# Performance work log

Hardware: AMD Instinct MI355X
Metric: run time of the kernel (lower is better)

## Reference

```python
import jax, jax.numpy as jnp
import numpy as np

FACTOR = 5

def setup_inputs() -> dict:
    key = jax.random.key(0)
    kq, kk, kv, ki = jax.random.split(key, 4)
    B, L, H, D = 8, 2048, 8, 64
    u = FACTOR * int(np.ceil(np.log(L)))  # sample_k == n_top == 40
    return {
        "queries": jax.random.normal(kq, (B, L, H, D), dtype=jnp.float32),
        "keys": jax.random.normal(kk, (B, L, H, D), dtype=jnp.float32),
        "values": jax.random.normal(kv, (B, L, H, D), dtype=jnp.float32),
        "index_sample": jax.random.randint(ki, (L, u), 0, L, dtype=jnp.int32),
    }

def reference(queries, keys, values, index_sample):
    B, L, H, D = queries.shape
    # faithful to torch .view(B, H, -1, D) on contiguous tensors (a reshape, not a transpose)
    q = queries.reshape(B, H, L, D)
    k = keys.reshape(B, H, L, D)
    v = values.reshape(B, H, L, D)
    u = FACTOR * int(np.ceil(np.log(L)))  # U_part == u
    # --- _prob_QK: sample keys per query, score, pick top-u queries ---
    K_sample = k[:, :, index_sample, :]                      # [B,H,L,u,D] gather over L_K
    QK_sample = jnp.einsum('bhld,bhlsd->bhls', q, K_sample)  # [B,H,L,u]
    M = QK_sample.max(axis=-1) - QK_sample.sum(axis=-1) / L  # sparsity measure [B,H,L]
    M_top = jax.lax.top_k(M, u)[1]                           # [B,H,u] indices of active queries
    Q_reduce = jnp.take_along_axis(q, M_top[..., None], axis=2)  # [B,H,u,D]
    scores = jnp.einsum('bhud,bhld->bhul', Q_reduce, k)      # [B,H,u,L]
    scale = 1.0 / float(np.sqrt(D))
    attn = jax.nn.softmax(scores * scale, axis=-1)           # dropout is identity in eval
    context = jnp.einsum('bhul,bhld->bhud', attn, v)         # [B,H,u,D]
    return context, attn
```

## Files before the change

kernel.cpp:

```cpp
#include <hip/hip_runtime.h>
#include <math.h>

#define LSEQ 2048
#define DDIM 64
#define UU   40
#define NBH  64
#define CTX_ELEMS (NBH*UU*DDIM)

__global__ __launch_bounds__(256, 8) void k12_sample_m(
    const float* __restrict__ q, const float* __restrict__ k,
    const int* __restrict__ idxs, float* __restrict__ M, float* __restrict__ ctx) {
  int b = blockIdx.x;
  int bh = b & 63;
  int ltile = b >> 6;
  int t = threadIdx.x;
  int lid = t >> 4;
  int lane = t & 15;
  int l = ltile * 16 + lid;

  int gt = b * 256 + t;
  if (gt < CTX_ELEMS) ctx[gt] = 0.f;

  float4 qv = *(const float4*)(q + ((size_t)(bh * LSEQ + l)) * DDIM + lane * 4);
  const float* kbase = k + (size_t)bh * LSEQ * DDIM;
  const int4* ir = (const int4*)(idxs + l * UU);

  float mx = -INFINITY, sm = 0.f;
#pragma unroll 1
  for (int s4 = 0; s4 < UU / 4; ++s4) {
    int4 jv = ir[s4];
    float4 k0 = *(const float4*)(kbase + (size_t)jv.x * DDIM + lane * 4);
    float4 k1 = *(const float4*)(kbase + (size_t)jv.y * DDIM + lane * 4);
    float4 k2 = *(const float4*)(kbase + (size_t)jv.z * DDIM + lane * 4);
    float4 k3 = *(const float4*)(kbase + (size_t)jv.w * DDIM + lane * 4);
    float d0 = qv.x * k0.x + qv.y * k0.y + qv.z * k0.z + qv.w * k0.w;
    float d1 = qv.x * k1.x + qv.y * k1.y + qv.z * k1.z + qv.w * k1.w;
    float d2 = qv.x * k2.x + qv.y * k2.y + qv.z * k2.z + qv.w * k2.w;
    float d3 = qv.x * k3.x + qv.y * k3.y + qv.z * k3.z + qv.w * k3.w;
#pragma unroll
    for (int off = 1; off < 16; off <<= 1) {
      d0 += __shfl_xor(d0, off, 64);
      d1 += __shfl_xor(d1, off, 64);
      d2 += __shfl_xor(d2, off, 64);
      d3 += __shfl_xor(d3, off, 64);
    }
    mx = fmaxf(fmaxf(fmaxf(mx, d0), fmaxf(d1, d2)), d3);
    sm += (d0 + d1) + (d2 + d3);
  }
  if (lane == 0) M[bh * LSEQ + l] = mx - sm * (1.0f / (float)LSEQ);
}

__global__ __launch_bounds__(256) void k3_topk(const float* __restrict__ M,
                                               int* __restrict__ Mtop) {
  int bh = blockIdx.x;
  int t = threadIdx.x;
  int w = t >> 6;
  int lane = t & 63;
  float v[8];
#pragma unroll
  for (int j = 0; j < 8; ++j) v[j] = M[bh * LSEQ + t + 256 * j];
  __shared__ float swv[4];
  __shared__ int   swi[4];
  __shared__ int   win;
  for (int it = 0; it < UU; ++it) {
    float bv = -INFINITY; int bi = 0x7fffffff;
#pragma unroll
    for (int j = 0; j < 8; ++j) {
      if (v[j] > bv) { bv = v[j]; bi = t + 256 * j; }
    }
#pragma unroll
    for (int off = 32; off > 0; off >>= 1) {
      float ov = __shfl_xor(bv, off, 64);
      int   oi = __shfl_xor(bi, off, 64);
      if (ov > bv || (ov == bv && oi < bi)) { bv = ov; bi = oi; }
    }
    if (lane == 0) { swv[w] = bv; swi[w] = bi; }
    __syncthreads();
    if (t == 0) {
      float fv = swv[0]; int fi = swi[0];
#pragma unroll
      for (int j = 1; j < 4; ++j) {
        if (swv[j] > fv || (swv[j] == fv && swi[j] < fi)) { fv = swv[j]; fi = swi[j]; }
      }
      Mtop[bh * UU + it] = fi;
      win = fi;
    }
    __syncthreads();
    int wi = win;
    if ((wi & 255) == t) v[wi >> 8] = -INFINITY;
  }
}

__global__ __launch_bounds__(256, 4) void k4_scores(
    const float* __restrict__ q, const float* __restrict__ k,
    const int* __restrict__ Mtop, float* __restrict__ attn) {
  int b = blockIdx.x;
  int bh = b & 63;
  int chunk = (b >> 6) & 7;
  int u0 = (b >> 9) * 20;
  int l = chunk * 256 + threadIdx.x;
  const float4* kr = (const float4*)(k + (size_t)(bh * LSEQ + l) * DDIM);
  float4 kv[16];
#pragma unroll
  for (int i = 0; i < 16; ++i) kv[i] = kr[i];
  for (int u = u0; u < u0 + 20; ++u) {
    int qi = __builtin_amdgcn_readfirstlane(Mtop[bh * UU + u]);
    const float4* qr = (const float4*)(q + (size_t)(bh * LSEQ + qi) * DDIM);
    float a0 = 0.f, a1 = 0.f, a2 = 0.f, a3 = 0.f;
#pragma unroll
    for (int i = 0; i < 16; i += 4) {
      float4 x0 = qr[i], x1 = qr[i+1], x2 = qr[i+2], x3 = qr[i+3];
      float4 y0 = kv[i], y1 = kv[i+1], y2 = kv[i+2], y3 = kv[i+3];
      a0 += x0.x*y0.x + x0.y*y0.y + x0.z*y0.z + x0.w*y0.w;
      a1 += x1.x*y1.x + x1.y*y1.y + x1.z*y1.z + x1.w*y1.w;
      a2 += x2.x*y2.x + x2.y*y2.y + x2.z*y2.z + x2.w*y2.w;
      a3 += x3.x*y3.x + x3.y*y3.y + x3.z*y3.z + x3.w*y3.w;
    }
    attn[(size_t)(bh * UU + u) * LSEQ + l] = ((a0+a1)+(a2+a3)) * 0.125f;
  }
}

__global__ __launch_bounds__(256) void k5_softmax(float* __restrict__ attn) {
  __shared__ float red[256];
  int row = blockIdx.x;
  float* p = attn + (size_t)row * LSEQ;
  int t = threadIdx.x;
  float v[8];
  float mx = -INFINITY;
#pragma unroll
  for (int i = 0; i < 8; ++i) { v[i] = p[t + 256 * i]; mx = fmaxf(mx, v[i]); }
  red[t] = mx; __syncthreads();
  for (int off = 128; off > 0; off >>= 1) {
    if (t < off) red[t] = fmaxf(red[t], red[t + off]);
    __syncthreads();
  }
  mx = red[0]; __syncthreads();
  float sm = 0.f;
#pragma unroll
  for (int i = 0; i < 8; ++i) { v[i] = __expf(v[i] - mx); sm += v[i]; }
  red[t] = sm; __syncthreads();
  for (int off = 128; off > 0; off >>= 1) {
    if (t < off) red[t] += red[t + off];
    __syncthreads();
  }
  float inv = 1.0f / red[0];
#pragma unroll
  for (int i = 0; i < 8; ++i) p[t + 256 * i] = v[i] * inv;
}

__global__ __launch_bounds__(256) void k7_context(
    const float* __restrict__ attn, const float* __restrict__ v,
    float* __restrict__ ctx) {
  __shared__ float vt[256 * DDIM];
  int b = blockIdx.x;
  int bh = b & 63;
  int l0 = (b >> 6) * 256;
  int t = threadIdx.x;

  const float4* src = (const float4*)(v + ((size_t)bh * LSEQ + l0) * DDIM);
  float4* dst = (float4*)vt;
#pragma unroll
  for (int i = 0; i < 16; ++i) dst[t + 256 * i] = src[t + 256 * i];
  __syncthreads();

  int w = t >> 6;
  int d = t & 63;
  const float* ab = attn + ((size_t)bh * UU + w * 10) * LSEQ + l0;
  float acc[10];
#pragma unroll
  for (int u = 0; u < 10; ++u) acc[u] = 0.f;
#pragma unroll 1
  for (int l4 = 0; l4 < 64; ++l4) {
    int l = l4 * 4;
    float4 av[10];
#pragma unroll
    for (int u = 0; u < 10; ++u)
      av[u] = *(const float4*)(ab + (size_t)u * LSEQ + l);
#pragma unroll
    for (int i = 0; i < 4; ++i) {
      float vv = vt[(l + i) * DDIM + d];
#pragma unroll
      for (int u = 0; u < 10; ++u)
        acc[u] = fmaf(((const float*)&av[u])[i], vv, acc[u]);
    }
  }
#pragma unroll
  for (int u = 0; u < 10; ++u)
    atomicAdd(&ctx[((size_t)bh * UU + w * 10 + u) * DDIM + d], acc[u]);
}

extern "C" void kernel_launch(void* const* d_in, const int* in_sizes, int n_in,
                              void* d_out, int out_size, void* d_ws, size_t ws_size,
                              hipStream_t stream) {
  const float* q   = (const float*)d_in[0];
  const float* k   = (const float*)d_in[1];
  const float* v   = (const float*)d_in[2];
  const int*   idx = (const int*)d_in[3];

  float* ctx  = (float*)d_out;
  float* attn = (float*)d_out + CTX_ELEMS;

  float* M    = (float*)d_ws;
  int*   Mtop = (int*)(M + NBH * LSEQ);

  k12_sample_m<<<NBH * 128, 256, 0, stream>>>(q, k, idx, M, ctx);
  k3_topk<<<NBH, 256, 0, stream>>>(M, Mtop);
  k4_scores<<<NBH * 16, 256, 0, stream>>>(q, k, Mtop, attn);
  k5_softmax<<<NBH * UU, 256, 0, stream>>>(attn);
  k7_context<<<NBH * 8, 256, 0, stream>>>(attn, v, ctx);
}
```

Measured before the change: 312.3 us.

## Fuse scores, softmax and context into one kernel using LDS-resident scores

```diff
diff --git a/kernel.cpp b/kernel.cpp
--- a/kernel.cpp
+++ b/kernel.cpp
@@ -9,7 +9,7 @@
 
 __global__ __launch_bounds__(256, 8) void k12_sample_m(
     const float* __restrict__ q, const float* __restrict__ k,
-    const int* __restrict__ idxs, float* __restrict__ M, float* __restrict__ ctx) {
+    const int* __restrict__ idxs, float* __restrict__ M) {
   int b = blockIdx.x;
   int bh = b & 63;
   int ltile = b >> 6;
@@ -17,9 +17,6 @@
   int lid = t >> 4;
   int lane = t & 15;
   int l = ltile * 16 + lid;
-
-  int gt = b * 256 + t;
-  if (gt < CTX_ELEMS) ctx[gt] = 0.f;
 
   float4 qv = *(const float4*)(q + ((size_t)(bh * LSEQ + l)) * DDIM + lane * 4);
   const float* kbase = k + (size_t)bh * LSEQ * DDIM;
@@ -91,102 +88,193 @@
   }
 }
 
-__global__ __launch_bounds__(256, 4) void k4_scores(
+__global__ __launch_bounds__(256, 2) void k457_fused(
     const float* __restrict__ q, const float* __restrict__ k,
-    const int* __restrict__ Mtop, float* __restrict__ attn) {
+    const float* __restrict__ v, const int* __restrict__ Mtop,
+    float* __restrict__ attn, float* __restrict__ ctx) {
+  __shared__ float sct[LSEQ * 8];
+  __shared__ float red[32 * 64];
+  __shared__ float stats[8];
   int b = blockIdx.x;
   int bh = b & 63;
-  int chunk = (b >> 6) & 7;
-  int u0 = (b >> 9) * 20;
-  int l = chunk * 256 + threadIdx.x;
-  const float4* kr = (const float4*)(k + (size_t)(bh * LSEQ + l) * DDIM);
-  float4 kv[16];
-#pragma unroll
-  for (int i = 0; i < 16; ++i) kv[i] = kr[i];
-  for (int u = u0; u < u0 + 20; ++u) {
-    int qi = __builtin_amdgcn_readfirstlane(Mtop[bh * UU + u]);
-    const float4* qr = (const float4*)(q + (size_t)(bh * LSEQ + qi) * DDIM);
-    float a0 = 0.f, a1 = 0.f, a2 = 0.f, a3 = 0.f;
-#pragma unroll
-    for (int i = 0; i < 16; i += 4) {
-      float4 x0 = qr[i], x1 = qr[i+1], x2 = qr[i+2], x3 = qr[i+3];
-      float4 y0 = kv[i], y1 = kv[i+1], y2 = kv[i+2], y3 = kv[i+3];
-      a0 += x0.x*y0.x + x0.y*y0.y + x0.z*y0.z + x0.w*y0.w;
-      a1 += x1.x*y1.x + x1.y*y1.y + x1.z*y1.z + x1.w*y1.w;
-      a2 += x2.x*y2.x + x2.y*y2.y + x2.z*y2.z + x2.w*y2.w;
-      a3 += x3.x*y3.x + x3.y*y3.y + x3.z*y3.z + x3.w*y3.w;
-    }
-    attn[(size_t)(bh * UU + u) * LSEQ + l] = ((a0+a1)+(a2+a3)) * 0.125f;
-  }
-}
-
-__global__ __launch_bounds__(256) void k5_softmax(float* __restrict__ attn) {
-  __shared__ float red[256];
-  int row = blockIdx.x;
-  float* p = attn + (size_t)row * LSEQ;
+  int ug = b >> 6;
+  int u0 = ug * 8;
   int t = threadIdx.x;
-  float v[8];
-  float mx = -INFINITY;
-#pragma unroll
-  for (int i = 0; i < 8; ++i) { v[i] = p[t + 256 * i]; mx = fmaxf(mx, v[i]); }
-  red[t] = mx; __syncthreads();
-  for (int off = 128; off > 0; off >>= 1) {
-    if (t < off) red[t] = fmaxf(red[t], red[t + off]);
-    __syncthreads();
-  }
-  mx = red[0]; __syncthreads();
-  float sm = 0.f;
-#pragma unroll
-  for (int i = 0; i < 8; ++i) { v[i] = __expf(v[i] - mx); sm += v[i]; }
-  red[t] = sm; __syncthreads();
-  for (int off = 128; off > 0; off >>= 1) {
-    if (t < off) red[t] += red[t + off];
-    __syncthreads();
-  }
-  float inv = 1.0f / red[0];
-#pragma unroll
-  for (int i = 0; i < 8; ++i) p[t + 256 * i] = v[i] * inv;
-}
-
-__global__ __launch_bounds__(256) void k7_context(
-    const float* __restrict__ attn, const float* __restrict__ v,
-    float* __restrict__ ctx) {
-  __shared__ float vt[256 * DDIM];
-  int b = blockIdx.x;
-  int bh = b & 63;
-  int l0 = (b >> 6) * 256;
-  int t = threadIdx.x;
-
-  const float4* src = (const float4*)(v + ((size_t)bh * LSEQ + l0) * DDIM);
-  float4* dst = (float4*)vt;
-#pragma unroll
-  for (int i = 0; i < 16; ++i) dst[t + 256 * i] = src[t + 256 * i];
-  __syncthreads();
-
-  int w = t >> 6;
-  int d = t & 63;
-  const float* ab = attn + ((size_t)bh * UU + w * 10) * LSEQ + l0;
-  float acc[10];
-#pragma unroll
-  for (int u = 0; u < 10; ++u) acc[u] = 0.f;
+  int w = t >> 6, lane = t & 63, g = lane >> 4, sub = lane & 15;
+
+  float4 qv[8];
+#pragma unroll
+  for (int u = 0; u < 8; ++u) {
+    int qi = Mtop[bh * UU + u0 + u];
+    qv[u] = *(const float4*)(q + ((size_t)(bh * LSEQ) + qi) * DDIM + sub * 4);
+  }
+
+  const float* kb = k + (size_t)bh * LSEQ * DDIM;
+  int lbase = w * 512 + g;
 #pragma unroll 1
-  for (int l4 = 0; l4 < 64; ++l4) {
-    int l = l4 * 4;
-    float4 av[10];
-#pragma unroll
-    for (int u = 0; u < 10; ++u)
-      av[u] = *(const float4*)(ab + (size_t)u * LSEQ + l);
-#pragma unroll
-    for (int i = 0; i < 4; ++i) {
-      float vv = vt[(l + i) * DDIM + d];
-#pragma unroll
-      for (int u = 0; u < 10; ++u)
-        acc[u] = fmaf(((const float*)&av[u])[i], vv, acc[u]);
-    }
-  }
-#pragma unroll
-  for (int u = 0; u < 10; ++u)
-    atomicAdd(&ctx[((size_t)bh * UU + w * 10 + u) * DDIM + d], acc[u]);
+  for (int i = 0; i < 128; ++i) {
+    int l = lbase + i * 4;
+    float4 kv = *(const float4*)(kb + (size_t)l * DDIM + sub * 4);
+    float d[8];
+#pragma unroll
+    for (int u = 0; u < 8; ++u) {
+      float s = qv[u].x * kv.x + qv[u].y * kv.y + qv[u].z * kv.z + qv[u].w * kv.w;
+#pragma unroll
+      for (int off = 1; off < 16; off <<= 1) s += __shfl_xor(s, off, 64);
+      d[u] = s * 0.125f;
+    }
+    if (sub == 0) {
+      *(float4*)&sct[l * 8]     = make_float4(d[0], d[1], d[2], d[3]);
+      *(float4*)&sct[l * 8 + 4] = make_float4(d[4], d[5], d[6], d[7]);
+    }
+  }
+  __syncthreads();
+
+  float4 ma = make_float4(-INFINITY, -INFINITY, -INFINITY, -INFINITY);
+  float4 mb = ma;
+#pragma unroll
+  for (int i = 0; i < 8; ++i) {
+    int l = t + 256 * i;
+    float4 a = *(float4*)&sct[l * 8];
+    float4 bb = *(float4*)&sct[l * 8 + 4];
+    ma.x = fmaxf(ma.x, a.x);  ma.y = fmaxf(ma.y, a.y);
+    ma.z = fmaxf(ma.z, a.z);  ma.w = fmaxf(ma.w, a.w);
+    mb.x = fmaxf(mb.x, bb.x); mb.y = fmaxf(mb.y, bb.y);
+    mb.z = fmaxf(mb.z, bb.z); mb.w = fmaxf(mb.w, bb.w);
+  }
+#pragma unroll
+  for (int off = 32; off > 0; off >>= 1) {
+    ma.x = fmaxf(ma.x, __shfl_xor(ma.x, off, 64));
+    ma.y = fmaxf(ma.y, __shfl_xor(ma.y, off, 64));
+    ma.z = fmaxf(ma.z, __shfl_xor(ma.z, off, 64));
+    ma.w = fmaxf(ma.w, __shfl_xor(ma.w, off, 64));
+    mb.x = fmaxf(mb.x, __shfl_xor(mb.x, off, 64));
+    mb.y = fmaxf(mb.y, __shfl_xor(mb.y, off, 64));
+    mb.z = fmaxf(mb.z, __shfl_xor(mb.z, off, 64));
+    mb.w = fmaxf(mb.w, __shfl_xor(mb.w, off, 64));
+  }
+  if (lane == 0) { *(float4*)&red[w * 8] = ma; *(float4*)&red[w * 8 + 4] = mb; }
+  __syncthreads();
+  {
+    float4 r0 = *(float4*)&red[0],  r1 = *(float4*)&red[8];
+    float4 r2 = *(float4*)&red[16], r3 = *(float4*)&red[24];
+    ma.x = fmaxf(fmaxf(r0.x, r1.x), fmaxf(r2.x, r3.x));
+    ma.y = fmaxf(fmaxf(r0.y, r1.y), fmaxf(r2.y, r3.y));
+    ma.z = fmaxf(fmaxf(r0.z, r1.z), fmaxf(r2.z, r3.z));
+    ma.w = fmaxf(fmaxf(r0.w, r1.w), fmaxf(r2.w, r3.w));
+    r0 = *(float4*)&red[4];  r1 = *(float4*)&red[12];
+    r2 = *(float4*)&red[20]; r3 = *(float4*)&red[28];
+    mb.x = fmaxf(fmaxf(r0.x, r1.x), fmaxf(r2.x, r3.x));
+    mb.y = fmaxf(fmaxf(r0.y, r1.y), fmaxf(r2.y, r3.y));
+    mb.z = fmaxf(fmaxf(r0.z, r1.z), fmaxf(r2.z, r3.z));
+    mb.w = fmaxf(fmaxf(r0.w, r1.w), fmaxf(r2.w, r3.w));
+  }
+  float4 sa = make_float4(0.f, 0.f, 0.f, 0.f), sb = sa;
+#pragma unroll
+  for (int i = 0; i < 8; ++i) {
+    int l = t + 256 * i;
+    float4 a = *(float4*)&sct[l * 8];
+    float4 bb = *(float4*)&sct[l * 8 + 4];
+    a.x = __expf(a.x - ma.x);  a.y = __expf(a.y - ma.y);
+    a.z = __expf(a.z - ma.z);  a.w = __expf(a.w - ma.w);
+    bb.x = __expf(bb.x - mb.x); bb.y = __expf(bb.y - mb.y);
+    bb.z = __expf(bb.z - mb.z); bb.w = __expf(bb.w - mb.w);
+    *(float4*)&sct[l * 8]     = a;
+    *(float4*)&sct[l * 8 + 4] = bb;
+    sa.x += a.x; sa.y += a.y; sa.z += a.z; sa.w += a.w;
+    sb.x += bb.x; sb.y += bb.y; sb.z += bb.z; sb.w += bb.w;
+  }
+#pragma unroll
+  for (int off = 32; off > 0; off >>= 1) {
+    sa.x += __shfl_xor(sa.x, off, 64); sa.y += __shfl_xor(sa.y, off, 64);
+    sa.z += __shfl_xor(sa.z, off, 64); sa.w += __shfl_xor(sa.w, off, 64);
+    sb.x += __shfl_xor(sb.x, off, 64); sb.y += __shfl_xor(sb.y, off, 64);
+    sb.z += __shfl_xor(sb.z, off, 64); sb.w += __shfl_xor(sb.w, off, 64);
+  }
+  if (lane == 0) { *(float4*)&red[64 + w * 8] = sa; *(float4*)&red[64 + w * 8 + 4] = sb; }
+  __syncthreads();
+  float4 inva, invb;
+  {
+    float4 r0 = *(float4*)&red[64],  r1 = *(float4*)&red[72];
+    float4 r2 = *(float4*)&red[80], r3 = *(float4*)&red[88];
+    inva.x = 1.0f / (r0.x + r1.x + r2.x + r3.x);
+    inva.y = 1.0f / (r0.y + r1.y + r2.y + r3.y);
+    inva.z = 1.0f / (r0.z + r1.z + r2.z + r3.z);
+    inva.w = 1.0f / (r0.w + r1.w + r2.w + r3.w);
+    r0 = *(float4*)&red[68];  r1 = *(float4*)&red[76];
+    r2 = *(float4*)&red[84]; r3 = *(float4*)&red[92];
+    invb.x = 1.0f / (r0.x + r1.x + r2.x + r3.x);
+    invb.y = 1.0f / (r0.y + r1.y + r2.y + r3.y);
+    invb.z = 1.0f / (r0.z + r1.z + r2.z + r3.z);
+    invb.w = 1.0f / (r0.w + r1.w + r2.w + r3.w);
+  }
+  if (t == 0) {
+    stats[0] = inva.x; stats[1] = inva.y; stats[2] = inva.z; stats[3] = inva.w;
+    stats[4] = invb.x; stats[5] = invb.y; stats[6] = invb.z; stats[7] = invb.w;
+  }
+
+  float* ap0 = attn + (size_t)(bh * UU + u0) * LSEQ;
+#pragma unroll
+  for (int i = 0; i < 8; ++i) {
+    int l = t + 256 * i;
+    float4 a = *(float4*)&sct[l * 8];
+    float4 bb = *(float4*)&sct[l * 8 + 4];
+    ap0[0 * LSEQ + l] = a.x * inva.x;
+    ap0[1 * LSEQ + l] = a.y * inva.y;
+    ap0[2 * LSEQ + l] = a.z * inva.z;
+    ap0[3 * LSEQ + l] = a.w * inva.w;
+    ap0[4 * LSEQ + l] = bb.x * invb.x;
+    ap0[5 * LSEQ + l] = bb.y * invb.y;
+    ap0[6 * LSEQ + l] = bb.z * invb.z;
+    ap0[7 * LSEQ + l] = bb.w * invb.w;
+  }
+  __syncthreads();
+
+  const float* vb = v + (size_t)bh * LSEQ * DDIM;
+  float4 acc[8];
+#pragma unroll
+  for (int u = 0; u < 8; ++u) acc[u] = make_float4(0.f, 0.f, 0.f, 0.f);
+#pragma unroll 1
+  for (int i = 0; i < 128; ++i) {
+    int l = lbase + i * 4;
+    float4 vv = *(const float4*)(vb + (size_t)l * DDIM + sub * 4);
+    float4 pa = *(float4*)&sct[l * 8];
+    float4 pb = *(float4*)&sct[l * 8 + 4];
+    float p[8] = {pa.x, pa.y, pa.z, pa.w, pb.x, pb.y, pb.z, pb.w};
+#pragma unroll
+    for (int u = 0; u < 8; ++u) {
+      acc[u].x = fmaf(p[u], vv.x, acc[u].x);
+      acc[u].y = fmaf(p[u], vv.y, acc[u].y);
+      acc[u].z = fmaf(p[u], vv.z, acc[u].z);
+      acc[u].w = fmaf(p[u], vv.w, acc[u].w);
+    }
+  }
+#pragma unroll
+  for (int off = 16; off <= 32; off <<= 1) {
+#pragma unroll
+    for (int u = 0; u < 8; ++u) {
+      acc[u].x += __shfl_xor(acc[u].x, off, 64);
+      acc[u].y += __shfl_xor(acc[u].y, off, 64);
+      acc[u].z += __shfl_xor(acc[u].z, off, 64);
+      acc[u].w += __shfl_xor(acc[u].w, off, 64);
+    }
+  }
+  if (g == 0) {
+#pragma unroll
+    for (int u = 0; u < 8; ++u)
+      *(float4*)&red[(w * 8 + u) * 64 + sub * 4] = acc[u];
+  }
+  __syncthreads();
+  {
+    int d = lane;
+#pragma unroll
+    for (int j = 0; j < 2; ++j) {
+      int u = (t >> 6) + j * 4;
+      float s = red[(0 * 8 + u) * 64 + d] + red[(1 * 8 + u) * 64 + d] +
+                red[(2 * 8 + u) * 64 + d] + red[(3 * 8 + u) * 64 + d];
+      ctx[(size_t)(bh * UU + u0 + u) * DDIM + d] = s * stats[u];
+    }
+  }
 }
 
 extern "C" void kernel_launch(void* const* d_in, const int* in_sizes, int n_in,
@@ -203,9 +291,7 @@
   float* M    = (float*)d_ws;
   int*   Mtop = (int*)(M + NBH * LSEQ);
 
-  k12_sample_m<<<NBH * 128, 256, 0, stream>>>(q, k, idx, M, ctx);
+  k12_sample_m<<<NBH * 128, 256, 0, stream>>>(q, k, idx, M);
   k3_topk<<<NBH, 256, 0, stream>>>(M, Mtop);
-  k4_scores<<<NBH * 16, 256, 0, stream>>>(q, k, Mtop, attn);
-  k5_softmax<<<NBH * UU, 256, 0, stream>>>(attn);
-  k7_context<<<NBH * 8, 256, 0, stream>>>(attn, v, ctx);
-}
+  k457_fused<<<NBH * 5, 256, 0, stream>>>(q, k, v, Mtop, attn, ctx);
+}
```

Result: slower. 386.1 us (+23.7%).

## Fuse scores and softmax via LDS rows; remap sample kernel to 4 lanes per query

Applied to the files above, without the earlier changes.

```diff
diff --git a/kernel.cpp b/kernel.cpp
--- a/kernel.cpp
+++ b/kernel.cpp
@@ -7,21 +7,22 @@
 #define NBH  64
 #define CTX_ELEMS (NBH*UU*DDIM)
 
-__global__ __launch_bounds__(256, 8) void k12_sample_m(
+__global__ __launch_bounds__(256, 4) void k12_sample_m(
     const float* __restrict__ q, const float* __restrict__ k,
-    const int* __restrict__ idxs, float* __restrict__ M, float* __restrict__ ctx) {
+    const int* __restrict__ idxs, float* __restrict__ M) {
   int b = blockIdx.x;
   int bh = b & 63;
   int ltile = b >> 6;
   int t = threadIdx.x;
-  int lid = t >> 4;
-  int lane = t & 15;
-  int l = ltile * 16 + lid;
-
-  int gt = b * 256 + t;
-  if (gt < CTX_ELEMS) ctx[gt] = 0.f;
-
-  float4 qv = *(const float4*)(q + ((size_t)(bh * LSEQ + l)) * DDIM + lane * 4);
+  int g = t >> 2;
+  int sub = t & 3;
+  int l = ltile * 64 + g;
+
+  const float4* qr = (const float4*)(q + (size_t)(bh * LSEQ + l) * DDIM);
+  float4 qv[4];
+#pragma unroll
+  for (int m = 0; m < 4; ++m) qv[m] = qr[4 * m + sub];
+
   const float* kbase = k + (size_t)bh * LSEQ * DDIM;
   const int4* ir = (const int4*)(idxs + l * UU);
 
@@ -29,25 +30,43 @@
 #pragma unroll 1
   for (int s4 = 0; s4 < UU / 4; ++s4) {
     int4 jv = ir[s4];
-    float4 k0 = *(const float4*)(kbase + (size_t)jv.x * DDIM + lane * 4);
-    float4 k1 = *(const float4*)(kbase + (size_t)jv.y * DDIM + lane * 4);
-    float4 k2 = *(const float4*)(kbase + (size_t)jv.z * DDIM + lane * 4);
-    float4 k3 = *(const float4*)(kbase + (size_t)jv.w * DDIM + lane * 4);
-    float d0 = qv.x * k0.x + qv.y * k0.y + qv.z * k0.z + qv.w * k0.w;
-    float d1 = qv.x * k1.x + qv.y * k1.y + qv.z * k1.z + qv.w * k1.w;
-    float d2 = qv.x * k2.x + qv.y * k2.y + qv.z * k2.z + qv.w * k2.w;
-    float d3 = qv.x * k3.x + qv.y * k3.y + qv.z * k3.z + qv.w * k3.w;
-#pragma unroll
-    for (int off = 1; off < 16; off <<= 1) {
-      d0 += __shfl_xor(d0, off, 64);
-      d1 += __shfl_xor(d1, off, 64);
-      d2 += __shfl_xor(d2, off, 64);
-      d3 += __shfl_xor(d3, off, 64);
-    }
+    const float4* k0 = (const float4*)(kbase + (size_t)jv.x * DDIM);
+    const float4* k1 = (const float4*)(kbase + (size_t)jv.y * DDIM);
+    const float4* k2 = (const float4*)(kbase + (size_t)jv.z * DDIM);
+    const float4* k3 = (const float4*)(kbase + (size_t)jv.w * DDIM);
+    float d0 = 0.f, d1 = 0.f, d2 = 0.f, d3 = 0.f;
+#pragma unroll
+    for (int m = 0; m < 4; ++m) {
+      float4 a = k0[4 * m + sub];
+      float4 x = qv[m];
+      d0 += x.x * a.x + x.y * a.y + x.z * a.z + x.w * a.w;
+    }
+#pragma unroll
+    for (int m = 0; m < 4; ++m) {
+      float4 a = k1[4 * m + sub];
+      float4 x = qv[m];
+      d1 += x.x * a.x + x.y * a.y + x.z * a.z + x.w * a.w;
+    }
+#pragma unroll
+    for (int m = 0; m < 4; ++m) {
+      float4 a = k2[4 * m + sub];
+      float4 x = qv[m];
+      d2 += x.x * a.x + x.y * a.y + x.z * a.z + x.w * a.w;
+    }
+#pragma unroll
+    for (int m = 0; m < 4; ++m) {
+      float4 a = k3[4 * m + sub];
+      float4 x = qv[m];
+      d3 += x.x * a.x + x.y * a.y + x.z * a.z + x.w * a.w;
+    }
+    d0 += __shfl_xor(d0, 1, 64); d0 += __shfl_xor(d0, 2, 64);
+    d1 += __shfl_xor(d1, 1, 64); d1 += __shfl_xor(d1, 2, 64);
+    d2 += __shfl_xor(d2, 1, 64); d2 += __shfl_xor(d2, 2, 64);
+    d3 += __shfl_xor(d3, 1, 64); d3 += __shfl_xor(d3, 2, 64);
     mx = fmaxf(fmaxf(fmaxf(mx, d0), fmaxf(d1, d2)), d3);
     sm += (d0 + d1) + (d2 + d3);
   }
-  if (lane == 0) M[bh * LSEQ + l] = mx - sm * (1.0f / (float)LSEQ);
+  if (sub == 0) M[bh * LSEQ + l] = mx - sm * (1.0f / (float)LSEQ);
 }
 
 __global__ __launch_bounds__(256) void k3_topk(const float* __restrict__ M,
@@ -91,61 +110,74 @@
   }
 }
 
-__global__ __launch_bounds__(256, 4) void k4_scores(
+__global__ __launch_bounds__(256, 4) void k45_scores_softmax(
     const float* __restrict__ q, const float* __restrict__ k,
-    const int* __restrict__ Mtop, float* __restrict__ attn) {
+    const int* __restrict__ Mtop, float* __restrict__ attn,
+    float* __restrict__ ctx) {
+  __shared__ float sct[4 * LSEQ];
   int b = blockIdx.x;
   int bh = b & 63;
-  int chunk = (b >> 6) & 7;
-  int u0 = (b >> 9) * 20;
-  int l = chunk * 256 + threadIdx.x;
-  const float4* kr = (const float4*)(k + (size_t)(bh * LSEQ + l) * DDIM);
-  float4 kv[16];
-#pragma unroll
-  for (int i = 0; i < 16; ++i) kv[i] = kr[i];
-  for (int u = u0; u < u0 + 20; ++u) {
-    int qi = __builtin_amdgcn_readfirstlane(Mtop[bh * UU + u]);
+  int u0 = (b >> 6) * 4;
+  int t = threadIdx.x;
+  int g = t >> 2;
+  int sub = t & 3;
+
+  ctx[b * 256 + t] = 0.f;
+
+  float4 qv[4][4];
+#pragma unroll
+  for (int u = 0; u < 4; ++u) {
+    int qi = Mtop[bh * UU + u0 + u];
     const float4* qr = (const float4*)(q + (size_t)(bh * LSEQ + qi) * DDIM);
-    float a0 = 0.f, a1 = 0.f, a2 = 0.f, a3 = 0.f;
-#pragma unroll
-    for (int i = 0; i < 16; i += 4) {
-      float4 x0 = qr[i], x1 = qr[i+1], x2 = qr[i+2], x3 = qr[i+3];
-      float4 y0 = kv[i], y1 = kv[i+1], y2 = kv[i+2], y3 = kv[i+3];
-      a0 += x0.x*y0.x + x0.y*y0.y + x0.z*y0.z + x0.w*y0.w;
-      a1 += x1.x*y1.x + x1.y*y1.y + x1.z*y1.z + x1.w*y1.w;
-      a2 += x2.x*y2.x + x2.y*y2.y + x2.z*y2.z + x2.w*y2.w;
-      a3 += x3.x*y3.x + x3.y*y3.y + x3.z*y3.z + x3.w*y3.w;
-    }
-    attn[(size_t)(bh * UU + u) * LSEQ + l] = ((a0+a1)+(a2+a3)) * 0.125f;
-  }
-}
-
-__global__ __launch_bounds__(256) void k5_softmax(float* __restrict__ attn) {
-  __shared__ float red[256];
-  int row = blockIdx.x;
-  float* p = attn + (size_t)row * LSEQ;
-  int t = threadIdx.x;
-  float v[8];
+#pragma unroll
+    for (int m = 0; m < 4; ++m) qv[u][m] = qr[4 * m + sub];
+  }
+
+  const float* kb = k + (size_t)bh * LSEQ * DDIM;
+#pragma unroll 1
+  for (int p = 0; p < 32; ++p) {
+    int l = p * 64 + g;
+    const float4* kr = (const float4*)(kb + (size_t)l * DDIM);
+    float4 ks[4];
+#pragma unroll
+    for (int m = 0; m < 4; ++m) ks[m] = kr[4 * m + sub];
+    float d[4];
+#pragma unroll
+    for (int u = 0; u < 4; ++u) {
+      float s = 0.f;
+#pragma unroll
+      for (int m = 0; m < 4; ++m) {
+        float4 x = qv[u][m], a = ks[m];
+        s += x.x * a.x + x.y * a.y + x.z * a.z + x.w * a.w;
+      }
+      s += __shfl_xor(s, 1, 64);
+      s += __shfl_xor(s, 2, 64);
+      d[u] = s * 0.125f;
+    }
+    if (sub == 0) {
+#pragma unroll
+      for (int u = 0; u < 4; ++u) sct[u * LSEQ + l] = d[u];
+    }
+  }
+  __syncthreads();
+
+  int w = t >> 6, lane = t & 63;
+  float* row = sct + w * LSEQ;
+  float vv[32];
   float mx = -INFINITY;
 #pragma unroll
-  for (int i = 0; i < 8; ++i) { v[i] = p[t + 256 * i]; mx = fmaxf(mx, v[i]); }
-  red[t] = mx; __syncthreads();
-  for (int off = 128; off > 0; off >>= 1) {
-    if (t < off) red[t] = fmaxf(red[t], red[t + off]);
-    __syncthreads();
-  }
-  mx = red[0]; __syncthreads();
+  for (int j = 0; j < 32; ++j) { vv[j] = row[lane + 64 * j]; mx = fmaxf(mx, vv[j]); }
+#pragma unroll
+  for (int off = 32; off > 0; off >>= 1) mx = fmaxf(mx, __shfl_xor(mx, off, 64));
   float sm = 0.f;
 #pragma unroll
-  for (int i = 0; i < 8; ++i) { v[i] = __expf(v[i] - mx); sm += v[i]; }
-  red[t] = sm; __syncthreads();
-  for (int off = 128; off > 0; off >>= 1) {
-    if (t < off) red[t] += red[t + off];
-    __syncthreads();
-  }
-  float inv = 1.0f / red[0];
-#pragma unroll
-  for (int i = 0; i < 8; ++i) p[t + 256 * i] = v[i] * inv;
+  for (int j = 0; j < 32; ++j) { vv[j] = __expf(vv[j] - mx); sm += vv[j]; }
+#pragma unroll
+  for (int off = 32; off > 0; off >>= 1) sm += __shfl_xor(sm, off, 64);
+  float inv = 1.0f / sm;
+  float* ap = attn + (size_t)(bh * UU + u0 + w) * LSEQ;
+#pragma unroll
+  for (int j = 0; j < 32; ++j) ap[lane + 64 * j] = vv[j] * inv;
 }
 
 __global__ __launch_bounds__(256) void k7_context(
@@ -178,10 +210,10 @@
       av[u] = *(const float4*)(ab + (size_t)u * LSEQ + l);
 #pragma unroll
     for (int i = 0; i < 4; ++i) {
-      float vv = vt[(l + i) * DDIM + d];
+      float vvv = vt[(l + i) * DDIM + d];
 #pragma unroll
       for (int u = 0; u < 10; ++u)
-        acc[u] = fmaf(((const float*)&av[u])[i], vv, acc[u]);
+        acc[u] = fmaf(((const float*)&av[u])[i], vvv, acc[u]);
     }
   }
 #pragma unroll
@@ -203,9 +235,8 @@
   float* M    = (float*)d_ws;
   int*   Mtop = (int*)(M + NBH * LSEQ);
 
-  k12_sample_m<<<NBH * 128, 256, 0, stream>>>(q, k, idx, M, ctx);
+  k12_sample_m<<<NBH * 32, 256, 0, stream>>>(q, k, idx, M);
   k3_topk<<<NBH, 256, 0, stream>>>(M, Mtop);
-  k4_scores<<<NBH * 16, 256, 0, stream>>>(q, k, Mtop, attn);
-  k5_softmax<<<NBH * UU, 256, 0, stream>>>(attn);
+  k45_scores_softmax<<<NBH * 10, 256, 0, stream>>>(q, k, Mtop, attn, ctx);
   k7_context<<<NBH * 8, 256, 0, stream>>>(attn, v, ctx);
 }
```

Measured after the change: 303.9 us. 1.03x faster.
